# Kernel tuning notes

Measured on AMD Instinct MI355X. Metric: run time of the kernel, lower is better.

Reference implementation:

```python
import jax, jax.numpy as jnp
import numpy as np

N_HEAD = 16

def setup_inputs() -> dict:
    key = jax.random.key(0)
    ks = jax.random.split(key, 8)
    B, Sq, Sk, D = 4, 1024, 2048, 1024
    s = 0.02  # GPT-2 init scale for weights
    return {
        "x": jax.random.normal(ks[0], (B, Sq, D), jnp.float32),
        "ctx": jax.random.normal(ks[1], (B, Sk, D), jnp.float32),
        "attention_mask": jnp.zeros((B, 1, 1, Sk), jnp.float32),
        "Wq": jax.random.normal(ks[2], (D, D), jnp.float32) * s,
        "bq": jnp.zeros((D,), jnp.float32),
        "Wkv": jax.random.normal(ks[3], (D, 2 * D), jnp.float32) * s,
        "bkv": jnp.zeros((2 * D,), jnp.float32),
        "Wp": jax.random.normal(ks[4], (D, D), jnp.float32) * s,
        "bp": jnp.zeros((D,), jnp.float32),
    }

def _split_heads(t):
    # [B, S, D] -> [B, H, S, dh]
    B, S, D = t.shape
    return t.reshape(B, S, N_HEAD, D // N_HEAD).transpose(0, 2, 1, 3)

def reference(x, ctx, attention_mask, Wq, bq, Wkv, bkv, Wp, bp):
    B, Sq, D = x.shape
    dh = D // N_HEAD
    q = _split_heads(x @ Wq + bq)                       # [B,H,Sq,dh]
    kv = ctx @ Wkv + bkv                                # [B,Sk,2D]
    k = _split_heads(kv[..., :D])                       # [B,H,Sk,dh]
    v = _split_heads(kv[..., D:])                       # [B,H,Sk,dh]
    w = jnp.einsum("bhqd,bhkd->bhqk", q, k) / jnp.sqrt(jnp.float32(dh))
    w = w + attention_mask
    w = jax.nn.softmax(w, axis=-1)                      # attn_pdrop=0 -> no dropout
    a = jnp.einsum("bhqk,bhkd->bhqd", w, v)             # [B,H,Sq,dh]
    a = a.transpose(0, 2, 1, 3).reshape(B, Sq, D)       # merge heads
    return a @ Wp + bp                                  # resid_pdrop=0
```

## Files before the change

kernel.cpp:

```cpp
#include <hip/hip_runtime.h>
#include <stdint.h>

#define H_B  4
#define H_SQ 1024
#define H_SK 2048
#define H_D  1024
#define H_NH 16
#define H_DH 64

typedef __bf16 bf16x8 __attribute__((ext_vector_type(8)));
typedef float  f32x4  __attribute__((ext_vector_type(4)));

__device__ __forceinline__ uint16_t f2bf(float f) {
    union { float f; uint32_t u; } v; v.f = f;
    uint32_t r = v.u + 0x7fffu + ((v.u >> 16) & 1u);
    return (uint16_t)(r >> 16);
}

__device__ __forceinline__ void gload_lds16(const void* g, void* l) {
    __builtin_amdgcn_global_load_lds(
        (const __attribute__((address_space(1))) uint32_t*)g,
        (__attribute__((address_space(3))) uint32_t*)l, 16, 0, 0);
}

#define MFMA_BF16(a, b, c) __builtin_amdgcn_mfma_f32_16x16x32_bf16((a), (b), (c), 0, 0, 0)
#define EXP2(x) __builtin_amdgcn_exp2f(x)

template <int CTRL>
__device__ __forceinline__ float dpp_xor(float v) {
    return __builtin_bit_cast(float,
        __builtin_amdgcn_update_dpp(__builtin_bit_cast(int, v),
                                    __builtin_bit_cast(int, v),
                                    CTRL, 0xF, 0xF, false));
}
#define DPP_XOR1 0xB1
#define DPP_XOR2 0x4E
#define DPP_XOR4 0x141
#define DPP_XOR8 0x140

__device__ __forceinline__ float dpp_max16(float v) {
    v = fmaxf(v, dpp_xor<DPP_XOR1>(v));
    v = fmaxf(v, dpp_xor<DPP_XOR2>(v));
    v = fmaxf(v, dpp_xor<DPP_XOR4>(v));
    v = fmaxf(v, dpp_xor<DPP_XOR8>(v));
    return v;
}
__device__ __forceinline__ float dpp_sum16(float v) {
    v += dpp_xor<DPP_XOR1>(v);
    v += dpp_xor<DPP_XOR2>(v);
    v += dpp_xor<DPP_XOR4>(v);
    v += dpp_xor<DPP_XOR8>(v);
    return v;
}

__global__ __launch_bounds__(256) void prep_kernel(
    const float* __restrict__ x, uint16_t* __restrict__ xb,
    const float* __restrict__ ctx, uint16_t* __restrict__ ctxb,
    const float* __restrict__ Wq, uint16_t* __restrict__ WqT,
    const float* __restrict__ Wkv, uint16_t* __restrict__ WkvT,
    const float* __restrict__ Wp, uint16_t* __restrict__ WpT)
{
    __shared__ float tile[32][33];
    int bid = blockIdx.x;
    int t = threadIdx.x;
    if (bid < 4096) {
        int bx = bid & 127, k0 = (bid >> 7) * 32;
        const float* W; uint16_t* WT; int N, n0;
        if (bx < 32)      { W = Wq;  WT = WqT;  N = 1024; n0 = bx * 32; }
        else if (bx < 96) { W = Wkv; WT = WkvT; N = 2048; n0 = (bx - 32) * 32; }
        else              { W = Wp;  WT = WpT;  N = 1024; n0 = (bx - 96) * 32; }
        int tx = t & 31, ty = t >> 5;
        #pragma unroll
        for (int i = ty; i < 32; i += 8)
            tile[i][tx] = W[(size_t)(k0 + i) * N + n0 + tx];
        __syncthreads();
        #pragma unroll
        for (int i = ty; i < 32; i += 8)
            WT[(size_t)(n0 + i) * 1024 + k0 + tx] = f2bf(tile[tx][i]);
    } else {
        const int n4a = (H_B * H_SQ * H_D) / 4;
        const int n4b = (H_B * H_SK * H_D) / 4;
        int i = (bid - 4096) * 256 + t;
        int stride = (gridDim.x - 4096) * 256;
        int tot = n4a + n4b;
        for (; i < tot; i += stride) {
            float4 v;
            if (i < n4a) v = ((const float4*)x)[i];
            else         v = ((const float4*)ctx)[i - n4a];
            ushort4 o;
            o.x = f2bf(v.x); o.y = f2bf(v.y); o.z = f2bf(v.z); o.w = f2bf(v.w);
            if (i < n4a) ((ushort4*)xb)[i] = o;
            else         ((ushort4*)ctxb)[i - n4a] = o;
        }
    }
}

template <int MODE, int BM>
__device__ __forceinline__ void gemm_body(
    const uint16_t* __restrict__ A, const uint16_t* __restrict__ BT,
    const float* __restrict__ bias, void* __restrict__ Cv,
    uint16_t* __restrict__ vTb, int M, int N, int K,
    int wg, int nwg, char* smem)
{
    constexpr int MI = BM / 32;
    uint16_t (*As)[BM * 32] = (uint16_t (*)[BM * 32])smem;
    uint16_t (*Bs)[128 * 32] = (uint16_t (*)[128 * 32])(smem + 2 * BM * 32 * 2);

    int nbn = N >> 7;
    int cpx = nwg >> 3;
    wg = (wg & 7) * cpx + (wg >> 3);
    int bm = wg / nbn, bn = wg % nbn;

    int t = threadIdx.x;
    int w = t >> 6, l = t & 63;
    int lr = l & 15, lg = l >> 4;
    int wr = (w >> 1) * (BM / 2), wc = (w & 1) * 64;

    const uint16_t* Ab = A + (size_t)bm * BM * K;
    const uint16_t* Bb = BT + (size_t)bn * 128 * K;

    int ca = w * 64 + l;
    int rowa = ca >> 2, kpa = (ca & 3) * 8;
    int cb = 256 + ca;
    int rowb = cb >> 2, kpb = (cb & 3) * 8;
    int offa = ca * 16;
    int offb = cb * 16;

    f32x4 acc[MI][4];
    #pragma unroll
    for (int i = 0; i < MI; ++i)
        #pragma unroll
        for (int j = 0; j < 4; ++j) acc[i][j] = {0.f, 0.f, 0.f, 0.f};

    gload_lds16(Ab + (size_t)rowa * K + kpa, (char*)As[0] + (offa & ~1023));
    if constexpr (BM == 128)
        gload_lds16(Ab + (size_t)rowb * K + kpb, (char*)As[0] + (offb & ~1023));
    gload_lds16(Bb + (size_t)rowa * K + kpa, (char*)Bs[0] + (offa & ~1023));
    gload_lds16(Bb + (size_t)rowb * K + kpb, (char*)Bs[0] + (offb & ~1023));
    __syncthreads();

    int buf = 0;
    for (int k0 = 0; k0 < K; k0 += 32) {
        if (k0 + 32 < K) {
            int kn = k0 + 32;
            gload_lds16(Ab + (size_t)rowa * K + kn + kpa, (char*)As[buf ^ 1] + (offa & ~1023));
            if constexpr (BM == 128)
                gload_lds16(Ab + (size_t)rowb * K + kn + kpb, (char*)As[buf ^ 1] + (offb & ~1023));
            gload_lds16(Bb + (size_t)rowa * K + kn + kpa, (char*)Bs[buf ^ 1] + (offa & ~1023));
            gload_lds16(Bb + (size_t)rowb * K + kn + kpb, (char*)Bs[buf ^ 1] + (offb & ~1023));
        }
        bf16x8 af[MI], bf[4];
        #pragma unroll
        for (int mi = 0; mi < MI; ++mi)
            af[mi] = *(const bf16x8*)&As[buf][(wr + mi * 16 + lr) * 32 + lg * 8];
        #pragma unroll
        for (int ni = 0; ni < 4; ++ni)
            bf[ni] = *(const bf16x8*)&Bs[buf][(wc + ni * 16 + lr) * 32 + lg * 8];
        #pragma unroll
        for (int mi = 0; mi < MI; ++mi)
            #pragma unroll
            for (int ni = 0; ni < 4; ++ni)
                acc[mi][ni] = MFMA_BF16(af[mi], bf[ni], acc[mi][ni]);
        __syncthreads();
        buf ^= 1;
    }

    #pragma unroll
    for (int mi = 0; mi < MI; ++mi) {
        #pragma unroll
        for (int ni = 0; ni < 4; ++ni) {
            int col = bn * 128 + wc + ni * 16 + lr;
            float bv = bias[col];
            int row0 = bm * BM + wr + mi * 16 + lg * 4;
            if constexpr (MODE == 2) {
                if (col < H_D) {
                    uint16_t* kb = (uint16_t*)Cv;
                    #pragma unroll
                    for (int j = 0; j < 4; ++j)
                        kb[(size_t)(row0 + j) * H_D + col] = f2bf(acc[mi][ni][j] + bv);
                } else {
                    int dall = col - H_D;
                    int hh = dall >> 6, dd = dall & 63;
                    int bb = row0 >> 11, sk0 = row0 & 2047;
                    uint16_t p0 = f2bf(acc[mi][ni][0] + bv);
                    uint16_t p1 = f2bf(acc[mi][ni][1] + bv);
                    uint16_t p2 = f2bf(acc[mi][ni][2] + bv);
                    uint16_t p3 = f2bf(acc[mi][ni][3] + bv);
                    uint32_t lo = (uint32_t)p0 | ((uint32_t)p1 << 16);
                    uint32_t hi = (uint32_t)p2 | ((uint32_t)p3 << 16);
                    *(uint2*)&vTb[((size_t)(bb * 16 + hh) * 64 + dd) * H_SK + sk0] =
                        make_uint2(lo, hi);
                }
            } else {
                #pragma unroll
                for (int j = 0; j < 4; ++j) {
                    float v = acc[mi][ni][j] + bv;
                    if constexpr (MODE == 0)
                        ((uint16_t*)Cv)[(size_t)(row0 + j) * N + col] = f2bf(v);
                    else
                        ((float*)Cv)[(size_t)(row0 + j) * N + col] = v;
                }
            }
        }
    }
}

__global__ __launch_bounds__(256) void qkv_gemm_kernel(
    const uint16_t* __restrict__ xb, const uint16_t* __restrict__ WqT,
    const float* __restrict__ bq, uint16_t* __restrict__ qb,
    const uint16_t* __restrict__ ctxb, const uint16_t* __restrict__ WkvT,
    const float* __restrict__ bkv, uint16_t* __restrict__ kb,
    uint16_t* __restrict__ vTb)
{
    __shared__ char smem[32768];
    int bid = blockIdx.x;
    if (bid < 512)
        gemm_body<0, 64>(xb, WqT, bq, qb, nullptr, H_B * H_SQ, H_D, H_D,
                         bid, 512, smem);
    else
        gemm_body<2, 128>(ctxb, WkvT, bkv, kb, vTb, H_B * H_SK, 2 * H_D, H_D,
                          bid - 512, 1024, smem);
}

__global__ __launch_bounds__(256) void proj_gemm_kernel(
    const uint16_t* __restrict__ ab, const uint16_t* __restrict__ WpT,
    const float* __restrict__ bp, float* __restrict__ out)
{
    __shared__ char smem[24576];
    gemm_body<1, 64>(ab, WpT, bp, out, nullptr, H_B * H_SQ, H_D, H_D,
                     blockIdx.x, 512, smem);
}

__global__ __launch_bounds__(256) void attn_kernel(
    const uint16_t* __restrict__ qb, const uint16_t* __restrict__ kb,
    const uint16_t* __restrict__ vT, const float* __restrict__ mask,
    uint16_t* __restrict__ ab)
{
    __shared__ uint16_t Ks[2][64 * 64];
    __shared__ uint16_t Vs[2][64 * 64];
    __shared__ uint16_t p_lds[4][16][64];

    int bid = blockIdx.x;
    int xcd = bid & 7;
    int kk = bid >> 3;
    int qt = kk & 15;
    int bh = xcd + 8 * (kk >> 4);
    int b = bh >> 4, hh = bh & 15;

    int t = threadIdx.x;
    int w = t >> 6, l = t & 63;
    int lr = l & 15, lg = l >> 4;

    const uint16_t* qrow = qb + (size_t)(b * H_SQ + qt * 64 + w * 16 + lr) * H_D + hh * H_DH;
    bf16x8 qf0 = *(const bf16x8*)(qrow + lg * 8);
    bf16x8 qf1 = *(const bf16x8*)(qrow + 32 + lg * 8);

    f32x4 acc[4];
    #pragma unroll
    for (int i = 0; i < 4; ++i) acc[i] = {0.f, 0.f, 0.f, 0.f};
    float mrow[4], lsum[4];
    #pragma unroll
    for (int j = 0; j < 4; ++j) { mrow[j] = -1e30f; lsum[j] = 0.f; }

    const float SC  = 0.18033688011112042f;
    const float L2E = 1.4426950408889634f;

    int c0 = w * 64 + l;
    int r0 = c0 >> 3,          gc0 = ((c0 & 7) ^ (r0 & 7)) * 8;
    int c1 = 256 + c0;
    int r1 = c1 >> 3,          gc1 = ((c1 & 7) ^ (r1 & 7)) * 8;
    int ldsoff = (w * 64) * 16;
    const uint16_t* kbase = kb + (size_t)b * H_SK * H_D + hh * H_DH;
    const uint16_t* vbase = vT + (size_t)bh * H_DH * H_SK;

    int xkbase = (lg & 1) << 5;
    int rdkey  = (lr & 7) << 3;

    float msk_nxt[4];
    {
        gload_lds16(kbase + (size_t)r0 * H_D + gc0, (char*)Ks[0] + ldsoff);
        gload_lds16(kbase + (size_t)r1 * H_D + gc1, (char*)Ks[0] + ldsoff + 4096);
        gload_lds16(vbase + (size_t)r0 * H_SK + gc0, (char*)Vs[0] + ldsoff);
        gload_lds16(vbase + (size_t)r1 * H_SK + gc1, (char*)Vs[0] + ldsoff + 4096);
        #pragma unroll
        for (int ni = 0; ni < 4; ++ni) msk_nxt[ni] = mask[b * H_SK + ni * 16 + lr] * L2E;
    }
    __syncthreads();

    int cur = 0;
    for (int kt = 0; kt < H_SK / 64; ++kt) {
        float msk_cur[4];
        #pragma unroll
        for (int ni = 0; ni < 4; ++ni) msk_cur[ni] = msk_nxt[ni];

        if (kt + 1 < H_SK / 64) {
            int sk1 = (kt + 1) * 64;
            int nxt = cur ^ 1;
            gload_lds16(kbase + (size_t)(sk1 + r0) * H_D + gc0, (char*)Ks[nxt] + ldsoff);
            gload_lds16(kbase + (size_t)(sk1 + r1) * H_D + gc1, (char*)Ks[nxt] + ldsoff + 4096);
            gload_lds16(vbase + (size_t)r0 * H_SK + sk1 + gc0, (char*)Vs[nxt] + ldsoff);
            gload_lds16(vbase + (size_t)r1 * H_SK + sk1 + gc1, (char*)Vs[nxt] + ldsoff + 4096);
            #pragma unroll
            for (int ni = 0; ni < 4; ++ni) msk_nxt[ni] = mask[b * H_SK + sk1 + ni * 16 + lr] * L2E;
        }

        const uint16_t* Kb = Ks[cur];
        const uint16_t* Vb = Vs[cur];
        int sw = (lg ^ (lr & 7)) * 8;

        f32x4 s[4];
        #pragma unroll
        for (int ni = 0; ni < 4; ++ni) s[ni] = {0.f, 0.f, 0.f, 0.f};
        #pragma unroll
        for (int ni = 0; ni < 4; ++ni) {
            bf16x8 kf0 = *(const bf16x8*)&Kb[(ni * 16 + lr) * 64 + sw];
            bf16x8 kf1 = *(const bf16x8*)&Kb[(ni * 16 + lr) * 64 + (sw ^ 32)];
            s[ni] = MFMA_BF16(qf0, kf0, s[ni]);
            s[ni] = MFMA_BF16(qf1, kf1, s[ni]);
        }

        float lg2[4][4], mxl[4];
        #pragma unroll
        for (int j = 0; j < 4; ++j) {
            float a0 = fmaf(s[0][j], SC, msk_cur[0]);
            float a1 = fmaf(s[1][j], SC, msk_cur[1]);
            float a2 = fmaf(s[2][j], SC, msk_cur[2]);
            float a3 = fmaf(s[3][j], SC, msk_cur[3]);
            lg2[0][j] = a0; lg2[1][j] = a1; lg2[2][j] = a2; lg2[3][j] = a3;
            mxl[j] = fmaxf(fmaxf(a0, a1), fmaxf(a2, a3));
        }
        int grow = 0;
        #pragma unroll
        for (int j = 0; j < 4; ++j)
            grow |= (mxl[j] > mrow[j] + 8.0f) ? 1 : 0;
        if (__any(grow)) {
            #pragma unroll
            for (int j = 0; j < 4; ++j) {
                float mx = dpp_max16(mxl[j]);
                float nm = fmaxf(mrow[j], mx);
                float alpha = EXP2(mrow[j] - nm);
                mrow[j] = nm;
                lsum[j] *= alpha;
                #pragma unroll
                for (int ni = 0; ni < 4; ++ni) acc[ni][j] *= alpha;
            }
        }
        #pragma unroll
        for (int ni = 0; ni < 4; ++ni)
            #pragma unroll
            for (int j = 0; j < 4; ++j) {
                float p = EXP2(lg2[ni][j] - mrow[j]);
                lsum[j] += p;
                uint32_t pk;
                asm("v_cvt_pk_bf16_f32 %0, %1, %2" : "=v"(pk) : "v"(p), "v"(p));
                p_lds[w][lg * 4 + j][(ni * 16 + lr) ^ (xkbase | (j << 3))] = (uint16_t)pk;
            }

        int pc0 = (lg * 8) ^ rdkey;
        bf16x8 pf0 = *(const bf16x8*)&p_lds[w][lr][pc0];
        bf16x8 pf1 = *(const bf16x8*)&p_lds[w][lr][pc0 ^ 32];
        #pragma unroll
        for (int ni = 0; ni < 4; ++ni) {
            bf16x8 vf0 = *(const bf16x8*)&Vb[(ni * 16 + lr) * 64 + sw];
            bf16x8 vf1 = *(const bf16x8*)&Vb[(ni * 16 + lr) * 64 + (sw ^ 32)];
            acc[ni] = MFMA_BF16(pf0, vf0, acc[ni]);
            acc[ni] = MFMA_BF16(pf1, vf1, acc[ni]);
        }

        __syncthreads();
        cur ^= 1;
    }

    float inv[4];
    #pragma unroll
    for (int j = 0; j < 4; ++j) inv[j] = 1.0f / dpp_sum16(lsum[j]);
    #pragma unroll
    for (int ni = 0; ni < 4; ++ni)
        #pragma unroll
        for (int j = 0; j < 4; ++j) {
            int row = qt * 64 + w * 16 + lg * 4 + j;
            int col = hh * H_DH + ni * 16 + lr;
            ab[(size_t)(b * H_SQ + row) * H_D + col] = f2bf(acc[ni][j] * inv[j]);
        }
}

extern "C" void kernel_launch(void* const* d_in, const int* in_sizes, int n_in,
                              void* d_out, int out_size, void* d_ws, size_t ws_size,
                              hipStream_t stream) {
    const float* x    = (const float*)d_in[0];
    const float* ctx  = (const float*)d_in[1];
    const float* mask = (const float*)d_in[2];
    const float* Wq   = (const float*)d_in[3];
    const float* bq   = (const float*)d_in[4];
    const float* Wkv  = (const float*)d_in[5];
    const float* bkv  = (const float*)d_in[6];
    const float* Wp   = (const float*)d_in[7];
    const float* bp   = (const float*)d_in[8];
    float* out = (float*)d_out;

    char* ws = (char*)d_ws;
    uint16_t* xb   = (uint16_t*)(ws + 0);
    uint16_t* ctxb = (uint16_t*)(ws + 8388608);
    uint16_t* vTb  = (uint16_t*)(ws + 25165824);
    uint16_t* WqT  = (uint16_t*)(ws + 41943040);
    uint16_t* WkvT = (uint16_t*)(ws + 44040192);
    uint16_t* WpT  = (uint16_t*)(ws + 48234496);
    uint16_t* qb   = (uint16_t*)(ws + 50331648);
    uint16_t* kb   = (uint16_t*)(ws + 58720256);
    uint16_t* ab   = xb;

    prep_kernel<<<7168, 256, 0, stream>>>(x, xb, ctx, ctxb, Wq, WqT, Wkv, WkvT, Wp, WpT);

    qkv_gemm_kernel<<<1536, 256, 0, stream>>>(xb, WqT, bq, qb, ctxb, WkvT, bkv, kb, vTb);

    attn_kernel<<<H_B * H_NH * (H_SQ / 64), 256, 0, stream>>>(qb, kb, vTb, mask, ab);

    proj_gemm_kernel<<<512, 256, 0, stream>>>(ab, WpT, bp, out);
}
```

Baseline: 168.8 us.

## Fuse fp32-to-bf16 activation conversion into QKV GEMM loads; raise MFMA priority

The separate pass that converted x and ctx to bf16 is removed. The QKV GEMM now reads fp32 activations straight from global memory into registers, converts them to bf16, and writes them to LDS after the MFMAs. This cuts out one full read-write round trip of 48 MB of activations. The cost is that the A operand no longer uses the async global-to-LDS path and needs more registers and VALU work inside the GEMM loop, since each A tile is now read at double width. The attention kernel also raises wave priority around its MFMA blocks with s_setprio.

```diff
diff --git a/kernel.cpp b/kernel.cpp
--- a/kernel.cpp
+++ b/kernel.cpp
@@ -54,8 +54,6 @@
 }
 
 __global__ __launch_bounds__(256) void prep_kernel(
-    const float* __restrict__ x, uint16_t* __restrict__ xb,
-    const float* __restrict__ ctx, uint16_t* __restrict__ ctxb,
     const float* __restrict__ Wq, uint16_t* __restrict__ WqT,
     const float* __restrict__ Wkv, uint16_t* __restrict__ WkvT,
     const float* __restrict__ Wp, uint16_t* __restrict__ WpT)
@@ -63,41 +61,24 @@
     __shared__ float tile[32][33];
     int bid = blockIdx.x;
     int t = threadIdx.x;
-    if (bid < 4096) {
-        int bx = bid & 127, k0 = (bid >> 7) * 32;
-        const float* W; uint16_t* WT; int N, n0;
-        if (bx < 32)      { W = Wq;  WT = WqT;  N = 1024; n0 = bx * 32; }
-        else if (bx < 96) { W = Wkv; WT = WkvT; N = 2048; n0 = (bx - 32) * 32; }
-        else              { W = Wp;  WT = WpT;  N = 1024; n0 = (bx - 96) * 32; }
-        int tx = t & 31, ty = t >> 5;
-        #pragma unroll
-        for (int i = ty; i < 32; i += 8)
-            tile[i][tx] = W[(size_t)(k0 + i) * N + n0 + tx];
-        __syncthreads();
-        #pragma unroll
-        for (int i = ty; i < 32; i += 8)
-            WT[(size_t)(n0 + i) * 1024 + k0 + tx] = f2bf(tile[tx][i]);
-    } else {
-        const int n4a = (H_B * H_SQ * H_D) / 4;
-        const int n4b = (H_B * H_SK * H_D) / 4;
-        int i = (bid - 4096) * 256 + t;
-        int stride = (gridDim.x - 4096) * 256;
-        int tot = n4a + n4b;
-        for (; i < tot; i += stride) {
-            float4 v;
-            if (i < n4a) v = ((const float4*)x)[i];
-            else         v = ((const float4*)ctx)[i - n4a];
-            ushort4 o;
-            o.x = f2bf(v.x); o.y = f2bf(v.y); o.z = f2bf(v.z); o.w = f2bf(v.w);
-            if (i < n4a) ((ushort4*)xb)[i] = o;
-            else         ((ushort4*)ctxb)[i - n4a] = o;
-        }
-    }
-}
-
-template <int MODE, int BM>
+    int bx = bid & 127, k0 = (bid >> 7) * 32;
+    const float* W; uint16_t* WT; int N, n0;
+    if (bx < 32)      { W = Wq;  WT = WqT;  N = 1024; n0 = bx * 32; }
+    else if (bx < 96) { W = Wkv; WT = WkvT; N = 2048; n0 = (bx - 32) * 32; }
+    else              { W = Wp;  WT = WpT;  N = 1024; n0 = (bx - 96) * 32; }
+    int tx = t & 31, ty = t >> 5;
+    #pragma unroll
+    for (int i = ty; i < 32; i += 8)
+        tile[i][tx] = W[(size_t)(k0 + i) * N + n0 + tx];
+    __syncthreads();
+    #pragma unroll
+    for (int i = ty; i < 32; i += 8)
+        WT[(size_t)(n0 + i) * 1024 + k0 + tx] = f2bf(tile[tx][i]);
+}
+
+template <int MODE, int BM, bool AF32>
 __device__ __forceinline__ void gemm_body(
-    const uint16_t* __restrict__ A, const uint16_t* __restrict__ BT,
+    const void* __restrict__ A, const uint16_t* __restrict__ BT,
     const float* __restrict__ bias, void* __restrict__ Cv,
     uint16_t* __restrict__ vTb, int M, int N, int K,
     int wg, int nwg, char* smem)
@@ -116,7 +97,10 @@
     int lr = l & 15, lg = l >> 4;
     int wr = (w >> 1) * (BM / 2), wc = (w & 1) * 64;
 
-    const uint16_t* Ab = A + (size_t)bm * BM * K;
+    const uint16_t* Ab16 = nullptr;
+    const float*    Abf  = nullptr;
+    if constexpr (AF32) Abf  = (const float*)A + (size_t)bm * BM * K;
+    else                Ab16 = (const uint16_t*)A + (size_t)bm * BM * K;
     const uint16_t* Bb = BT + (size_t)bn * 128 * K;
 
     int ca = w * 64 + l;
@@ -126,26 +110,57 @@
     int offa = ca * 16;
     int offb = cb * 16;
 
+    int rA0 = ca >> 2, kA0 = (ca & 3) * 8;
+    int rA1 = cb >> 2, kA1 = (cb & 3) * 8;
+
     f32x4 acc[MI][4];
     #pragma unroll
     for (int i = 0; i < MI; ++i)
         #pragma unroll
         for (int j = 0; j < 4; ++j) acc[i][j] = {0.f, 0.f, 0.f, 0.f};
 
-    gload_lds16(Ab + (size_t)rowa * K + kpa, (char*)As[0] + (offa & ~1023));
-    if constexpr (BM == 128)
-        gload_lds16(Ab + (size_t)rowb * K + kpb, (char*)As[0] + (offb & ~1023));
+    if constexpr (AF32) {
+        float4 u0 = *(const float4*)(Abf + (size_t)rA0 * K + kA0);
+        float4 v0 = *(const float4*)(Abf + (size_t)rA0 * K + kA0 + 4);
+        bf16x8 o0;
+        o0[0] = (__bf16)u0.x; o0[1] = (__bf16)u0.y; o0[2] = (__bf16)u0.z; o0[3] = (__bf16)u0.w;
+        o0[4] = (__bf16)v0.x; o0[5] = (__bf16)v0.y; o0[6] = (__bf16)v0.z; o0[7] = (__bf16)v0.w;
+        *(bf16x8*)((char*)As[0] + ca * 16) = o0;
+        if constexpr (BM == 128) {
+            float4 u1 = *(const float4*)(Abf + (size_t)rA1 * K + kA1);
+            float4 v1 = *(const float4*)(Abf + (size_t)rA1 * K + kA1 + 4);
+            bf16x8 o1;
+            o1[0] = (__bf16)u1.x; o1[1] = (__bf16)u1.y; o1[2] = (__bf16)u1.z; o1[3] = (__bf16)u1.w;
+            o1[4] = (__bf16)v1.x; o1[5] = (__bf16)v1.y; o1[6] = (__bf16)v1.z; o1[7] = (__bf16)v1.w;
+            *(bf16x8*)((char*)As[0] + cb * 16) = o1;
+        }
+    } else {
+        gload_lds16(Ab16 + (size_t)rowa * K + kpa, (char*)As[0] + (offa & ~1023));
+        if constexpr (BM == 128)
+            gload_lds16(Ab16 + (size_t)rowb * K + kpb, (char*)As[0] + (offb & ~1023));
+    }
     gload_lds16(Bb + (size_t)rowa * K + kpa, (char*)Bs[0] + (offa & ~1023));
     gload_lds16(Bb + (size_t)rowb * K + kpb, (char*)Bs[0] + (offb & ~1023));
     __syncthreads();
 
     int buf = 0;
     for (int k0 = 0; k0 < K; k0 += 32) {
-        if (k0 + 32 < K) {
+        bool pf = (k0 + 32 < K);
+        float4 u0{}, v0{}, u1{}, v1{};
+        if (pf) {
             int kn = k0 + 32;
-            gload_lds16(Ab + (size_t)rowa * K + kn + kpa, (char*)As[buf ^ 1] + (offa & ~1023));
-            if constexpr (BM == 128)
-                gload_lds16(Ab + (size_t)rowb * K + kn + kpb, (char*)As[buf ^ 1] + (offb & ~1023));
+            if constexpr (AF32) {
+                u0 = *(const float4*)(Abf + (size_t)rA0 * K + kn + kA0);
+                v0 = *(const float4*)(Abf + (size_t)rA0 * K + kn + kA0 + 4);
+                if constexpr (BM == 128) {
+                    u1 = *(const float4*)(Abf + (size_t)rA1 * K + kn + kA1);
+                    v1 = *(const float4*)(Abf + (size_t)rA1 * K + kn + kA1 + 4);
+                }
+            } else {
+                gload_lds16(Ab16 + (size_t)rowa * K + kn + kpa, (char*)As[buf ^ 1] + (offa & ~1023));
+                if constexpr (BM == 128)
+                    gload_lds16(Ab16 + (size_t)rowb * K + kn + kpb, (char*)As[buf ^ 1] + (offb & ~1023));
+            }
             gload_lds16(Bb + (size_t)rowa * K + kn + kpa, (char*)Bs[buf ^ 1] + (offa & ~1023));
             gload_lds16(Bb + (size_t)rowb * K + kn + kpb, (char*)Bs[buf ^ 1] + (offb & ~1023));
         }
@@ -161,6 +176,18 @@
             #pragma unroll
             for (int ni = 0; ni < 4; ++ni)
                 acc[mi][ni] = MFMA_BF16(af[mi], bf[ni], acc[mi][ni]);
+        if (AF32 && pf) {
+            bf16x8 o0;
+            o0[0] = (__bf16)u0.x; o0[1] = (__bf16)u0.y; o0[2] = (__bf16)u0.z; o0[3] = (__bf16)u0.w;
+            o0[4] = (__bf16)v0.x; o0[5] = (__bf16)v0.y; o0[6] = (__bf16)v0.z; o0[7] = (__bf16)v0.w;
+            *(bf16x8*)((char*)As[buf ^ 1] + ca * 16) = o0;
+            if constexpr (BM == 128) {
+                bf16x8 o1;
+                o1[0] = (__bf16)u1.x; o1[1] = (__bf16)u1.y; o1[2] = (__bf16)u1.z; o1[3] = (__bf16)u1.w;
+                o1[4] = (__bf16)v1.x; o1[5] = (__bf16)v1.y; o1[6] = (__bf16)v1.z; o1[7] = (__bf16)v1.w;
+                *(bf16x8*)((char*)As[buf ^ 1] + cb * 16) = o1;
+            }
+        }
         __syncthreads();
         buf ^= 1;
     }
@@ -206,20 +233,20 @@
 }
 
 __global__ __launch_bounds__(256) void qkv_gemm_kernel(
-    const uint16_t* __restrict__ xb, const uint16_t* __restrict__ WqT,
+    const float* __restrict__ x, const uint16_t* __restrict__ WqT,
     const float* __restrict__ bq, uint16_t* __restrict__ qb,
-    const uint16_t* __restrict__ ctxb, const uint16_t* __restrict__ WkvT,
+    const float* __restrict__ ctx, const uint16_t* __restrict__ WkvT,
     const float* __restrict__ bkv, uint16_t* __restrict__ kb,
     uint16_t* __restrict__ vTb)
 {
     __shared__ char smem[32768];
     int bid = blockIdx.x;
     if (bid < 512)
-        gemm_body<0, 64>(xb, WqT, bq, qb, nullptr, H_B * H_SQ, H_D, H_D,
-                         bid, 512, smem);
+        gemm_body<0, 64, true>(x, WqT, bq, qb, nullptr, H_B * H_SQ, H_D, H_D,
+                               bid, 512, smem);
     else
-        gemm_body<2, 128>(ctxb, WkvT, bkv, kb, vTb, H_B * H_SK, 2 * H_D, H_D,
-                          bid - 512, 1024, smem);
+        gemm_body<2, 128, true>(ctx, WkvT, bkv, kb, vTb, H_B * H_SK, 2 * H_D, H_D,
+                                bid - 512, 1024, smem);
 }
 
 __global__ __launch_bounds__(256) void proj_gemm_kernel(
@@ -227,8 +254,8 @@
     const float* __restrict__ bp, float* __restrict__ out)
 {
     __shared__ char smem[24576];
-    gemm_body<1, 64>(ab, WpT, bp, out, nullptr, H_B * H_SQ, H_D, H_D,
-                     blockIdx.x, 512, smem);
+    gemm_body<1, 64, false>(ab, WpT, bp, out, nullptr, H_B * H_SQ, H_D, H_D,
+                            blockIdx.x, 512, smem);
 }
 
 __global__ __launch_bounds__(256) void attn_kernel(
@@ -311,6 +338,7 @@
         f32x4 s[4];
         #pragma unroll
         for (int ni = 0; ni < 4; ++ni) s[ni] = {0.f, 0.f, 0.f, 0.f};
+        __builtin_amdgcn_s_setprio(1);
         #pragma unroll
         for (int ni = 0; ni < 4; ++ni) {
             bf16x8 kf0 = *(const bf16x8*)&Kb[(ni * 16 + lr) * 64 + sw];
@@ -318,6 +346,7 @@
             s[ni] = MFMA_BF16(qf0, kf0, s[ni]);
             s[ni] = MFMA_BF16(qf1, kf1, s[ni]);
         }
+        __builtin_amdgcn_s_setprio(0);
 
         float lg2[4][4], mxl[4];
         #pragma unroll
@@ -359,6 +388,7 @@
         int pc0 = (lg * 8) ^ rdkey;
         bf16x8 pf0 = *(const bf16x8*)&p_lds[w][lr][pc0];
         bf16x8 pf1 = *(const bf16x8*)&p_lds[w][lr][pc0 ^ 32];
+        __builtin_amdgcn_s_setprio(1);
         #pragma unroll
         for (int ni = 0; ni < 4; ++ni) {
             bf16x8 vf0 = *(const bf16x8*)&Vb[(ni * 16 + lr) * 64 + sw];
@@ -366,6 +396,7 @@
             acc[ni] = MFMA_BF16(pf0, vf0, acc[ni]);
             acc[ni] = MFMA_BF16(pf1, vf1, acc[ni]);
         }
+        __builtin_amdgcn_s_setprio(0);
 
         __syncthreads();
         cur ^= 1;
@@ -399,19 +430,17 @@
     float* out = (float*)d_out;
 
     char* ws = (char*)d_ws;
-    uint16_t* xb   = (uint16_t*)(ws + 0);
-    uint16_t* ctxb = (uint16_t*)(ws + 8388608);
-    uint16_t* vTb  = (uint16_t*)(ws + 25165824);
-    uint16_t* WqT  = (uint16_t*)(ws + 41943040);
-    uint16_t* WkvT = (uint16_t*)(ws + 44040192);
-    uint16_t* WpT  = (uint16_t*)(ws + 48234496);
-    uint16_t* qb   = (uint16_t*)(ws + 50331648);
-    uint16_t* kb   = (uint16_t*)(ws + 58720256);
-    uint16_t* ab   = xb;
-
-    prep_kernel<<<7168, 256, 0, stream>>>(x, xb, ctx, ctxb, Wq, WqT, Wkv, WkvT, Wp, WpT);
-
-    qkv_gemm_kernel<<<1536, 256, 0, stream>>>(xb, WqT, bq, qb, ctxb, WkvT, bkv, kb, vTb);
+    uint16_t* ab   = (uint16_t*)(ws + 0);
+    uint16_t* vTb  = (uint16_t*)(ws + 8388608);
+    uint16_t* WqT  = (uint16_t*)(ws + 25165824);
+    uint16_t* WkvT = (uint16_t*)(ws + 27262976);
+    uint16_t* WpT  = (uint16_t*)(ws + 31457280);
+    uint16_t* qb   = (uint16_t*)(ws + 33554432);
+    uint16_t* kb   = (uint16_t*)(ws + 41943040);
+
+    prep_kernel<<<4096, 256, 0, stream>>>(Wq, WqT, Wkv, WkvT, Wp, WpT);
+
+    qkv_gemm_kernel<<<1536, 256, 0, stream>>>(x, WqT, bq, qb, ctx, WkvT, bkv, kb, vTb);
 
     attn_kernel<<<H_B * H_NH * (H_SQ / 64), 256, 0, stream>>>(qb, kb, vTb, mask, ab);
 
```

Result: slower. 196.4 us (+16.3%).
